# Performance work log

Measured on AMD Instinct MI355X. Metric: run time of the kernel, lower is better.

## Reference

```python
import jax, jax.numpy as jnp
import numpy as np

BIG = 1.0e6  # sentinel 'infinite' 1D distance (BIG**2 = 1e12 is safely finite in fp32)


def _edt_sq(zero_mask):
    """Exact squared Euclidean distance transform to nearest True in zero_mask.

    Two-pass separable exact EDT (matches scipy.ndimage.distance_transform_edt):
      pass 1: 1-D distance along W via forward/backward cummax scans
      pass 2: min-plus over H: D2[i,j] = min_k g2[k,j] + (i-k)^2
    zero_mask: [H, W] bool (True where the source array equals 0).
    """
    H, W = zero_mask.shape
    col = jnp.arange(W, dtype=jnp.float32)
    # index of last zero to the left / first zero to the right
    last = jax.lax.cummax(jnp.where(zero_mask, col, -BIG), axis=1)
    nxt = -jax.lax.cummax(jnp.where(zero_mask, -col, -BIG), axis=1, reverse=True)
    g = jnp.minimum(jnp.minimum(col - last, nxt - col), BIG)  # [H, W] 1-D dist
    g2 = g * g
    row = jnp.arange(H, dtype=jnp.float32)
    sq = (row[:, None] - row[None, :]) ** 2  # [H, H]
    # D2[i, j] = min_k g2[k, j] + (i - k)^2  -- exact 2-D squared EDT
    return jnp.min(g2[None, :, :] + sq[:, :, None], axis=1)


def _distance_map(mask):
    """Signed distance map: EDT(mask) - EDT(1 - mask); zeros if mask empty."""
    pos = jnp.sqrt(_edt_sq(mask == 0))   # dist of foreground px to nearest background
    neg = jnp.sqrt(_edt_sq(mask != 0))   # dist of background px to nearest foreground
    d = pos - neg
    return jnp.where(mask.sum() == 0, jnp.zeros_like(d), d)


def boundary_loss(pred, target):
    B, C, H, W = pred.shape
    masks = target.reshape(B * C, H, W)
    # sequence over B*C to keep the [H,H,W] min-plus intermediate per-image
    dmaps = jax.lax.map(_distance_map, masks).reshape(B, C, H, W)
    # sum_c mean_{b,h,w}(sig(pred_c)*d_c) / C  ==  overall mean
    return jnp.mean(jax.nn.sigmoid(pred) * dmaps)


def setup_inputs() -> dict:
    key = jax.random.key(0)
    k1, k2 = jax.random.split(key)
    pred = jax.random.normal(k1, (8, 3, 256, 256), dtype=jnp.float32)
    target = jax.random.randint(k2, (8, 3, 256, 256), 0, 2, dtype=jnp.int32)
    return {"pred": pred, "target": target}


def reference(pred, target):
    return boundary_loss(pred, target)
```

## Files before the change

kernel.cpp:

```cpp
#include <hip/hip_runtime.h>
#include <math.h>

#define NIMG 24
#define H    256
#define W    256
#define NPIX (H * W)
#define NROWS (NIMG * H)
#define CPB  8
#define LDP  9
#define GRID2 (NIMG * (W / CPB))
#define NPART GRID2
#define BIGI 1000000
#define BIGF 1.0e6f
#define CAPTHR (-5.0e5f)

__global__ void edt_rows_kernel(const int* __restrict__ tgt,
                                float* __restrict__ f) {
    const int tid  = blockIdx.x * 256 + threadIdx.x;
    const int gw   = tid >> 6;
    const int lane = tid & 63;
    const int img  = gw >> 8;
    const int row  = gw & 255;

    const int4 tv = ((const int4*)(tgt + (img << 16) + (row << 8)))[lane];
    const int c0 = lane << 2;

    const int prevw = __shfl_up(tv.w, 1, 64);
    const bool ch0 = (lane > 0) && ((tv.x != 0) != (prevw != 0));
    const bool ch1 = (tv.y != 0) != (tv.x != 0);
    const bool ch2 = (tv.z != 0) != (tv.y != 0);
    const bool ch3 = (tv.w != 0) != (tv.z != 0);

    const int a0 = ch0 ? c0     : -BIGI;
    const int a1 = ch1 ? c0 + 1 : a0;
    const int a2 = ch2 ? c0 + 2 : a1;
    const int a3 = ch3 ? c0 + 3 : a2;
    const int rb3 = ch3 ? c0 + 3 : BIGI;
    const int rb2 = ch2 ? c0 + 2 : rb3;
    const int rb1 = ch1 ? c0 + 1 : rb2;
    const int rb0 = ch0 ? c0     : rb1;

    const unsigned long long mask = __ballot(ch0 | ch1 | ch2 | ch3);
    const unsigned long long lowm = mask & ((1ULL << lane) - 1ULL);
    const unsigned long long him  = (lane < 63) ? (mask >> (lane + 1)) : 0ULL;

    const int plane = 63 - __builtin_clzll(lowm | 1ULL);
    const int sh_a  = __shfl(a3, plane & 63, 64);
    const int ex    = (lowm != 0ULL) ? sh_a : -BIGI;

    const int qlane = lane + 1 +
        (int)__builtin_ctzll(him | 0x8000000000000000ULL);
    const int sh_r  = __shfl(rb0, qlane & 63, 64);
    const int exr   = (him != 0ULL) ? sh_r : BIGI;

    const int s0 = (ex > a0) ? ex : a0;
    const int s1 = (ex > a1) ? ex : a1;
    const int s2 = (ex > a2) ? ex : a2;
    const int s3 = (ex > a3) ? ex : a3;
    const int n0 = (rb1 < exr) ? rb1 : exr;
    const int n1 = (rb2 < exr) ? rb2 : exr;
    const int n2 = (rb3 < exr) ? rb3 : exr;
    const int n3 = exr;

    auto gcalc = [](int c, int s, int n) -> int {
        int dp = c - s + 1;
        int dn = n - c;
        int g = dp < dn ? dp : dn;
        return g < BIGI ? g : BIGI;
    };
    const float g0 = (float)gcalc(c0,     s0, n0);
    const float g1 = (float)gcalc(c0 + 1, s1, n1);
    const float g2 = (float)gcalc(c0 + 2, s2, n2);
    const float g3 = (float)gcalc(c0 + 3, s3, n3);

    float4 o;
    o.x = (tv.x != 0) ? g0 : -g0;
    o.y = (tv.y != 0) ? g1 : -g1;
    o.z = (tv.z != 0) ? g2 : -g2;
    o.w = (tv.w != 0) ? g3 : -g3;
    ((float4*)(f + (img << 16) + (row << 8)))[lane] = o;
}

__global__ void edt_cols_kernel(const float* __restrict__ f,
                                const float* __restrict__ pred,
                                double* __restrict__ partials) {
    const int bid  = blockIdx.x;
    const int img  = bid >> 5;
    const int j0   = (bid & 31) << 3;
    const int t    = threadIdx.x;
    const int lane = t & 63;
    const int wid  = t >> 6;

    __shared__ float sf[H][LDP];
    __shared__ double wsum[4];
    __shared__ int nonempty;
    if (t == 0) nonempty = 0;
    __syncthreads();

    bool myne = false;
#pragma unroll
    for (int s = 0; s < 2; ++s) {
        const int id  = t + (s << 8);
        const int row = id >> 1;
        const int q   = (id & 1) << 2;
        const float4 v = *(const float4*)(f + (img << 16) + (row << 8) + j0 + q);
        sf[row][q]     = v.x;  sf[row][q + 1] = v.y;
        sf[row][q + 2] = v.z;  sf[row][q + 3] = v.w;
        myne = myne || (v.x > CAPTHR) || (v.y > CAPTHR) ||
                       (v.z > CAPTHR) || (v.w > CAPTHR);
    }
    if (myne) nonempty = 1;
    __syncthreads();
    const int flag = nonempty;

    const int c  = t & 7;
    const int r0 = (t >> 3) << 3;
    double acc = 0.0;
#pragma unroll
    for (int ii = 0; ii < 8; ++ii) {
        const int i = r0 + ii;
        const float fv = sf[i][c];
        const bool  m  = fv > 0.0f;
        const float sgn = m ? 1.0f : -1.0f;
        const float gi = fabsf(fv);
        const int  gii = (int)gi;
        int lo = i - gii; lo = lo > 0 ? lo : 0;
        int hi = i + gii; hi = hi < (H - 1) ? hi : (H - 1);

        float dm = 3.0e38f;
        float dk = (float)(i - lo);
        for (int k = lo; k <= hi; ++k) {
            const float g = fmaxf(sgn * sf[k][c], 0.0f);
            dm = fminf(dm, g * g + dk * dk);
            dk -= 1.0f;
        }

        float d = m ? sqrtf(dm) : -sqrtf(dm);
        if (!flag) d = 0.0f;
        const float p = pred[(img << 16) + (i << 8) + j0 + c];
        const float sig = 1.0f / (1.0f + expf(-p));
        acc += (double)sig * (double)d;
    }

#pragma unroll
    for (int off = 32; off > 0; off >>= 1) acc += __shfl_down(acc, off, 64);
    if (lane == 0) wsum[wid] = acc;
    __syncthreads();
    if (t == 0) partials[bid] = (wsum[0] + wsum[1]) + (wsum[2] + wsum[3]);
}

__global__ void finalize_kernel(const double* __restrict__ partials,
                                float* __restrict__ out) {
    const int t = threadIdx.x;
    double a = 0.0;
#pragma unroll
    for (int s = 0; s < NPART / 64; ++s) a += partials[t + (s << 6)];
#pragma unroll
    for (int off = 32; off > 0; off >>= 1) a += __shfl_down(a, off, 64);
    if (t == 0) out[0] = (float)(a / (double)(NIMG * NPIX));
}

extern "C" void kernel_launch(void* const* d_in, const int* in_sizes, int n_in,
                              void* d_out, int out_size, void* d_ws, size_t ws_size,
                              hipStream_t stream) {
    const float* pred = (const float*)d_in[0];
    const int*   tgt  = (const int*)d_in[1];
    float* out = (float*)d_out;

    char* ws = (char*)d_ws;
    const size_t fbytes = (size_t)NIMG * NPIX * sizeof(float);
    float*  fbuf     = (float*)(ws);
    double* partials = (double*)(ws + fbytes);

    edt_rows_kernel<<<NROWS / 4, 256, 0, stream>>>(tgt, fbuf);
    edt_cols_kernel<<<GRID2, 256, 0, stream>>>(fbuf, pred, partials);
    finalize_kernel<<<1, 64, 0, stream>>>(partials, out);
}
```

Before: 25.58 us.

## Fuse row EDT, column EDT and final reduction into one kernel with per-image barriers

Merges the three launches into one persistent-style kernel. Each block computes 8 rows of the row pass and writes them to global memory. It then waits on a per-image atomic counter barrier before running the column min-plus pass. The last block to finish does the final reduction, found through an atomic ticket. Pred is prefetched into shared memory before the barrier to hide its load latency. The aim is to remove launch overhead and inter-kernel gaps, at the cost of a memset launch, spin-wait barriers that need all 32 blocks of an image co-resident, and extra shared memory.

```diff
diff --git a/kernel.cpp b/kernel.cpp
--- a/kernel.cpp
+++ b/kernel.cpp
@@ -5,105 +5,126 @@
 #define H    256
 #define W    256
 #define NPIX (H * W)
-#define NROWS (NIMG * H)
+#define SLICES 32
+#define NBLK (NIMG * SLICES)
+#define BLKT 256
 #define CPB  8
 #define LDP  9
-#define GRID2 (NIMG * (W / CPB))
-#define NPART GRID2
 #define BIGI 1000000
-#define BIGF 1.0e6f
 #define CAPTHR (-5.0e5f)
 
-__global__ void edt_rows_kernel(const int* __restrict__ tgt,
-                                float* __restrict__ f) {
-    const int tid  = blockIdx.x * 256 + threadIdx.x;
-    const int gw   = tid >> 6;
-    const int lane = tid & 63;
-    const int img  = gw >> 8;
-    const int row  = gw & 255;
-
-    const int4 tv = ((const int4*)(tgt + (img << 16) + (row << 8)))[lane];
-    const int c0 = lane << 2;
-
-    const int prevw = __shfl_up(tv.w, 1, 64);
-    const bool ch0 = (lane > 0) && ((tv.x != 0) != (prevw != 0));
-    const bool ch1 = (tv.y != 0) != (tv.x != 0);
-    const bool ch2 = (tv.z != 0) != (tv.y != 0);
-    const bool ch3 = (tv.w != 0) != (tv.z != 0);
-
-    const int a0 = ch0 ? c0     : -BIGI;
-    const int a1 = ch1 ? c0 + 1 : a0;
-    const int a2 = ch2 ? c0 + 2 : a1;
-    const int a3 = ch3 ? c0 + 3 : a2;
-    const int rb3 = ch3 ? c0 + 3 : BIGI;
-    const int rb2 = ch2 ? c0 + 2 : rb3;
-    const int rb1 = ch1 ? c0 + 1 : rb2;
-    const int rb0 = ch0 ? c0     : rb1;
-
-    const unsigned long long mask = __ballot(ch0 | ch1 | ch2 | ch3);
-    const unsigned long long lowm = mask & ((1ULL << lane) - 1ULL);
-    const unsigned long long him  = (lane < 63) ? (mask >> (lane + 1)) : 0ULL;
-
-    const int plane = 63 - __builtin_clzll(lowm | 1ULL);
-    const int sh_a  = __shfl(a3, plane & 63, 64);
-    const int ex    = (lowm != 0ULL) ? sh_a : -BIGI;
-
-    const int qlane = lane + 1 +
-        (int)__builtin_ctzll(him | 0x8000000000000000ULL);
-    const int sh_r  = __shfl(rb0, qlane & 63, 64);
-    const int exr   = (him != 0ULL) ? sh_r : BIGI;
-
-    const int s0 = (ex > a0) ? ex : a0;
-    const int s1 = (ex > a1) ? ex : a1;
-    const int s2 = (ex > a2) ? ex : a2;
-    const int s3 = (ex > a3) ? ex : a3;
-    const int n0 = (rb1 < exr) ? rb1 : exr;
-    const int n1 = (rb2 < exr) ? rb2 : exr;
-    const int n2 = (rb3 < exr) ? rb3 : exr;
-    const int n3 = exr;
-
-    auto gcalc = [](int c, int s, int n) -> int {
-        int dp = c - s + 1;
-        int dn = n - c;
-        int g = dp < dn ? dp : dn;
-        return g < BIGI ? g : BIGI;
-    };
-    const float g0 = (float)gcalc(c0,     s0, n0);
-    const float g1 = (float)gcalc(c0 + 1, s1, n1);
-    const float g2 = (float)gcalc(c0 + 2, s2, n2);
-    const float g3 = (float)gcalc(c0 + 3, s3, n3);
-
-    float4 o;
-    o.x = (tv.x != 0) ? g0 : -g0;
-    o.y = (tv.y != 0) ? g1 : -g1;
-    o.z = (tv.z != 0) ? g2 : -g2;
-    o.w = (tv.w != 0) ? g3 : -g3;
-    ((float4*)(f + (img << 16) + (row << 8)))[lane] = o;
-}
-
-__global__ void edt_cols_kernel(const float* __restrict__ f,
-                                const float* __restrict__ pred,
-                                double* __restrict__ partials) {
+__global__ __launch_bounds__(BLKT)
+void boundary_fused_kernel(const int* __restrict__ tgt,
+                           const float* __restrict__ pred,
+                           float* __restrict__ fbuf,
+                           double* __restrict__ partials,
+                           unsigned int* __restrict__ syncw,
+                           float* __restrict__ out) {
     const int bid  = blockIdx.x;
     const int img  = bid >> 5;
-    const int j0   = (bid & 31) << 3;
+    const int grp  = bid & 31;
+    const int j0   = grp << 3;
     const int t    = threadIdx.x;
     const int lane = t & 63;
     const int wid  = t >> 6;
 
     __shared__ float sf[H][LDP];
+    __shared__ float sp[H][LDP];
     __shared__ double wsum[4];
-    __shared__ int nonempty;
+    __shared__ int nonempty, won;
     if (t == 0) nonempty = 0;
-    __syncthreads();
-
-    bool myne = false;
+
+#pragma unroll
+    for (int s = 0; s < 2; ++s) {
+        const int row = (grp << 3) + (wid << 1) + s;
+        const int4 tv = ((const int4*)(tgt + (img << 16) + (row << 8)))[lane];
+        const int c0 = lane << 2;
+
+        const int prevw = __shfl_up(tv.w, 1, 64);
+        const bool ch0 = (lane > 0) && ((tv.x != 0) != (prevw != 0));
+        const bool ch1 = (tv.y != 0) != (tv.x != 0);
+        const bool ch2 = (tv.z != 0) != (tv.y != 0);
+        const bool ch3 = (tv.w != 0) != (tv.z != 0);
+
+        const int a0 = ch0 ? c0     : -BIGI;
+        const int a1 = ch1 ? c0 + 1 : a0;
+        const int a2 = ch2 ? c0 + 2 : a1;
+        const int a3 = ch3 ? c0 + 3 : a2;
+        const int rb3 = ch3 ? c0 + 3 : BIGI;
+        const int rb2 = ch2 ? c0 + 2 : rb3;
+        const int rb1 = ch1 ? c0 + 1 : rb2;
+        const int rb0 = ch0 ? c0     : rb1;
+
+        const unsigned long long mask = __ballot(ch0 | ch1 | ch2 | ch3);
+        const unsigned long long lowm = mask & ((1ULL << lane) - 1ULL);
+        const unsigned long long him  = (lane < 63) ? (mask >> (lane + 1)) : 0ULL;
+
+        const int plane = 63 - __builtin_clzll(lowm | 1ULL);
+        const int sh_a  = __shfl(a3, plane & 63, 64);
+        const int ex    = (lowm != 0ULL) ? sh_a : -BIGI;
+
+        const int qlane = lane + 1 +
+            (int)__builtin_ctzll(him | 0x8000000000000000ULL);
+        const int sh_r  = __shfl(rb0, qlane & 63, 64);
+        const int exr   = (him != 0ULL) ? sh_r : BIGI;
+
+        const int s0 = (ex > a0) ? ex : a0;
+        const int s1 = (ex > a1) ? ex : a1;
+        const int s2 = (ex > a2) ? ex : a2;
+        const int s3 = (ex > a3) ? ex : a3;
+        const int n0 = (rb1 < exr) ? rb1 : exr;
+        const int n1 = (rb2 < exr) ? rb2 : exr;
+        const int n2 = (rb3 < exr) ? rb3 : exr;
+        const int n3 = exr;
+
+        auto gcalc = [](int c, int ss, int nn) -> int {
+            int dp = c - ss + 1;
+            int dn = nn - c;
+            int g = dp < dn ? dp : dn;
+            return g < BIGI ? g : BIGI;
+        };
+        const float g0 = (float)gcalc(c0,     s0, n0);
+        const float g1 = (float)gcalc(c0 + 1, s1, n1);
+        const float g2 = (float)gcalc(c0 + 2, s2, n2);
+        const float g3 = (float)gcalc(c0 + 3, s3, n3);
+
+        float4 o;
+        o.x = (tv.x != 0) ? g0 : -g0;
+        o.y = (tv.y != 0) ? g1 : -g1;
+        o.z = (tv.z != 0) ? g2 : -g2;
+        o.w = (tv.w != 0) ? g3 : -g3;
+        ((float4*)(fbuf + (img << 16) + (row << 8)))[lane] = o;
+    }
+
 #pragma unroll
     for (int s = 0; s < 2; ++s) {
         const int id  = t + (s << 8);
         const int row = id >> 1;
         const int q   = (id & 1) << 2;
-        const float4 v = *(const float4*)(f + (img << 16) + (row << 8) + j0 + q);
+        const float4 v = *(const float4*)(pred + (img << 16) + (row << 8) + j0 + q);
+        sp[row][q]     = v.x;  sp[row][q + 1] = v.y;
+        sp[row][q + 2] = v.z;  sp[row][q + 3] = v.w;
+    }
+
+    __syncthreads();
+    if (t == 0) {
+        __threadfence();
+        atomicAdd(&syncw[img << 4], 1u);
+        while (__hip_atomic_load(&syncw[img << 4], __ATOMIC_RELAXED,
+                                 __HIP_MEMORY_SCOPE_AGENT) < SLICES) {
+            __builtin_amdgcn_s_sleep(2);
+        }
+        __threadfence();
+    }
+    __syncthreads();
+
+    bool myne = false;
+#pragma unroll
+    for (int s = 0; s < 2; ++s) {
+        const int id  = t + (s << 8);
+        const int row = id >> 1;
+        const int q   = (id & 1) << 2;
+        const float4 v = *(const float4*)(fbuf + (img << 16) + (row << 8) + j0 + q);
         sf[row][q]     = v.x;  sf[row][q + 1] = v.y;
         sf[row][q + 2] = v.z;  sf[row][q + 3] = v.w;
         myne = myne || (v.x > CAPTHR) || (v.y > CAPTHR) ||
@@ -137,7 +158,7 @@
 
         float d = m ? sqrtf(dm) : -sqrtf(dm);
         if (!flag) d = 0.0f;
-        const float p = pred[(img << 16) + (i << 8) + j0 + c];
+        const float p = sp[i][c];
         const float sig = 1.0f / (1.0f + expf(-p));
         acc += (double)sig * (double)d;
     }
@@ -146,18 +167,23 @@
     for (int off = 32; off > 0; off >>= 1) acc += __shfl_down(acc, off, 64);
     if (lane == 0) wsum[wid] = acc;
     __syncthreads();
-    if (t == 0) partials[bid] = (wsum[0] + wsum[1]) + (wsum[2] + wsum[3]);
-}
-
-__global__ void finalize_kernel(const double* __restrict__ partials,
-                                float* __restrict__ out) {
-    const int t = threadIdx.x;
-    double a = 0.0;
-#pragma unroll
-    for (int s = 0; s < NPART / 64; ++s) a += partials[t + (s << 6)];
-#pragma unroll
-    for (int off = 32; off > 0; off >>= 1) a += __shfl_down(a, off, 64);
-    if (t == 0) out[0] = (float)(a / (double)(NIMG * NPIX));
+    if (t == 0) {
+        partials[bid] = (wsum[0] + wsum[1]) + (wsum[2] + wsum[3]);
+        __threadfence();
+        const unsigned old = atomicAdd(&syncw[NIMG << 4], 1u);
+        won = (old == (unsigned)(NBLK - 1));
+    }
+    __syncthreads();
+
+    if (won && t < 64) {
+        __threadfence();
+        double a = 0.0;
+#pragma unroll
+        for (int s = 0; s < NBLK / 64; ++s) a += partials[t + (s << 6)];
+#pragma unroll
+        for (int off = 32; off > 0; off >>= 1) a += __shfl_down(a, off, 64);
+        if (t == 0) out[0] = (float)(a / (double)(NIMG * NPIX));
+    }
 }
 
 extern "C" void kernel_launch(void* const* d_in, const int* in_sizes, int n_in,
@@ -169,10 +195,11 @@
 
     char* ws = (char*)d_ws;
     const size_t fbytes = (size_t)NIMG * NPIX * sizeof(float);
-    float*  fbuf     = (float*)(ws);
-    double* partials = (double*)(ws + fbytes);
-
-    edt_rows_kernel<<<NROWS / 4, 256, 0, stream>>>(tgt, fbuf);
-    edt_cols_kernel<<<GRID2, 256, 0, stream>>>(fbuf, pred, partials);
-    finalize_kernel<<<1, 64, 0, stream>>>(partials, out);
+    float*        fbuf     = (float*)(ws);
+    double*       partials = (double*)(ws + fbytes);
+    unsigned int* syncw    = (unsigned int*)(ws + fbytes + NBLK * sizeof(double));
+
+    hipMemsetAsync(syncw, 0, (NIMG + 1) * 64, stream);
+    boundary_fused_kernel<<<NBLK, BLKT, 0, stream>>>(tgt, pred, fbuf,
+                                                     partials, syncw, out);
 }
```

Result: slower. 90.64 us (+254.4%).

## Store row distances as int16 and fold final reduction into column kernel

Applied to the files above, without the earlier changes.

The row pass now writes signed 1-D distances as shorts, capping the no-zero case at a sentinel that the column kernel expands back to 1e6, so the intermediate buffer is half as large. The separate finalize launch is removed. The last finishing block, found through per-image and global atomic counters that the row kernel resets, now sums the partials. This cuts intermediate memory traffic and one kernel launch, at the cost of atomics and threadfences and a dependency on counter reset ordering between kernels.

```diff
diff --git a/kernel.cpp b/kernel.cpp
--- a/kernel.cpp
+++ b/kernel.cpp
@@ -7,15 +7,18 @@
 #define NPIX (H * W)
 #define NROWS (NIMG * H)
 #define CPB  8
+#define SLICES (W / CPB)
+#define NBLK2 (NIMG * SLICES)
 #define LDP  9
-#define GRID2 (NIMG * (W / CPB))
-#define NPART GRID2
 #define BIGI 1000000
-#define BIGF 1.0e6f
-#define CAPTHR (-5.0e5f)
+#define CAPS 1024
 
 __global__ void edt_rows_kernel(const int* __restrict__ tgt,
-                                float* __restrict__ f) {
+                                short* __restrict__ f,
+                                unsigned int* __restrict__ syncw) {
+    if (blockIdx.x == 0 && threadIdx.x <= NIMG)
+        syncw[threadIdx.x << 4] = 0;
+
     const int tid  = blockIdx.x * 256 + threadIdx.x;
     const int gw   = tid >> 6;
     const int lane = tid & 63;
@@ -62,28 +65,31 @@
     const int n2 = (rb3 < exr) ? rb3 : exr;
     const int n3 = exr;
 
-    auto gcalc = [](int c, int s, int n) -> int {
-        int dp = c - s + 1;
-        int dn = n - c;
+    auto gcalc = [](int c, int ss, int nn) -> int {
+        int dp = c - ss + 1;
+        int dn = nn - c;
         int g = dp < dn ? dp : dn;
-        return g < BIGI ? g : BIGI;
+        return (g < BIGI) ? g : CAPS;
     };
-    const float g0 = (float)gcalc(c0,     s0, n0);
-    const float g1 = (float)gcalc(c0 + 1, s1, n1);
-    const float g2 = (float)gcalc(c0 + 2, s2, n2);
-    const float g3 = (float)gcalc(c0 + 3, s3, n3);
+    const int g0 = gcalc(c0,     s0, n0);
+    const int g1 = gcalc(c0 + 1, s1, n1);
+    const int g2 = gcalc(c0 + 2, s2, n2);
+    const int g3 = gcalc(c0 + 3, s3, n3);
 
-    float4 o;
-    o.x = (tv.x != 0) ? g0 : -g0;
-    o.y = (tv.y != 0) ? g1 : -g1;
-    o.z = (tv.z != 0) ? g2 : -g2;
-    o.w = (tv.w != 0) ? g3 : -g3;
-    ((float4*)(f + (img << 16) + (row << 8)))[lane] = o;
+    short4 o;
+    o.x = (short)((tv.x != 0) ? g0 : -g0);
+    o.y = (short)((tv.y != 0) ? g1 : -g1);
+    o.z = (short)((tv.z != 0) ? g2 : -g2);
+    o.w = (short)((tv.w != 0) ? g3 : -g3);
+    ((short4*)(f + (img << 16) + (row << 8)))[lane] = o;
 }
 
-__global__ void edt_cols_kernel(const float* __restrict__ f,
-                                const float* __restrict__ pred,
-                                double* __restrict__ partials) {
+__global__ __launch_bounds__(256)
+void edt_cols_kernel(const short* __restrict__ f,
+                     const float* __restrict__ pred,
+                     double* __restrict__ partials,
+                     unsigned int* __restrict__ syncw,
+                     float* __restrict__ out) {
     const int bid  = blockIdx.x;
     const int img  = bid >> 5;
     const int j0   = (bid & 31) << 3;
@@ -93,23 +99,25 @@
 
     __shared__ float sf[H][LDP];
     __shared__ double wsum[4];
-    __shared__ int nonempty;
+    __shared__ int nonempty, won;
     if (t == 0) nonempty = 0;
     __syncthreads();
 
-    bool myne = false;
+    {
+        const int4 rv = *(const int4*)(f + (img << 16) + (t << 8) + j0);
+        const short* sv = (const short*)&rv;
+        bool ne = false;
 #pragma unroll
-    for (int s = 0; s < 2; ++s) {
-        const int id  = t + (s << 8);
-        const int row = id >> 1;
-        const int q   = (id & 1) << 2;
-        const float4 v = *(const float4*)(f + (img << 16) + (row << 8) + j0 + q);
-        sf[row][q]     = v.x;  sf[row][q + 1] = v.y;
-        sf[row][q + 2] = v.z;  sf[row][q + 3] = v.w;
-        myne = myne || (v.x > CAPTHR) || (v.y > CAPTHR) ||
-                       (v.z > CAPTHR) || (v.w > CAPTHR);
+        for (int j = 0; j < 8; ++j) {
+            const int v = sv[j];
+            ne = ne || (v != -CAPS);
+            float g = (float)v;
+            if (v == CAPS)  g =  1.0e6f;
+            if (v == -CAPS) g = -1.0e6f;
+            sf[t][j] = g;
+        }
+        if (ne) nonempty = 1;
     }
-    if (myne) nonempty = 1;
     __syncthreads();
     const int flag = nonempty;
 
@@ -146,18 +154,28 @@
     for (int off = 32; off > 0; off >>= 1) acc += __shfl_down(acc, off, 64);
     if (lane == 0) wsum[wid] = acc;
     __syncthreads();
-    if (t == 0) partials[bid] = (wsum[0] + wsum[1]) + (wsum[2] + wsum[3]);
-}
+    if (t == 0) {
+        partials[bid] = (wsum[0] + wsum[1]) + (wsum[2] + wsum[3]);
+        __threadfence();
+        int w = 0;
+        const unsigned o1 = atomicAdd(&syncw[img << 4], 1u);
+        if (o1 == (unsigned)(SLICES - 1)) {
+            const unsigned o2 = atomicAdd(&syncw[NIMG << 4], 1u);
+            w = (o2 == (unsigned)(NIMG - 1));
+        }
+        won = w;
+    }
+    __syncthreads();
 
-__global__ void finalize_kernel(const double* __restrict__ partials,
-                                float* __restrict__ out) {
-    const int t = threadIdx.x;
-    double a = 0.0;
+    if (won && t < 64) {
+        __threadfence();
+        double a = 0.0;
 #pragma unroll
-    for (int s = 0; s < NPART / 64; ++s) a += partials[t + (s << 6)];
+        for (int s = 0; s < NBLK2 / 64; ++s) a += partials[t + (s << 6)];
 #pragma unroll
-    for (int off = 32; off > 0; off >>= 1) a += __shfl_down(a, off, 64);
-    if (t == 0) out[0] = (float)(a / (double)(NIMG * NPIX));
+        for (int off = 32; off > 0; off >>= 1) a += __shfl_down(a, off, 64);
+        if (t == 0) out[0] = (float)(a / (double)(NIMG * NPIX));
+    }
 }
 
 extern "C" void kernel_launch(void* const* d_in, const int* in_sizes, int n_in,
@@ -168,11 +186,11 @@
     float* out = (float*)d_out;
 
     char* ws = (char*)d_ws;
-    const size_t fbytes = (size_t)NIMG * NPIX * sizeof(float);
-    float*  fbuf     = (float*)(ws);
-    double* partials = (double*)(ws + fbytes);
+    const size_t fbytes = (size_t)NIMG * NPIX * sizeof(short);
+    short*        fbuf     = (short*)(ws);
+    double*       partials = (double*)(ws + fbytes);
+    unsigned int* syncw    = (unsigned int*)(ws + fbytes + NBLK2 * sizeof(double));
 
-    edt_rows_kernel<<<NROWS / 4, 256, 0, stream>>>(tgt, fbuf);
-    edt_cols_kernel<<<GRID2, 256, 0, stream>>>(fbuf, pred, partials);
-    finalize_kernel<<<1, 64, 0, stream>>>(partials, out);
+    edt_rows_kernel<<<NROWS / 4, 256, 0, stream>>>(tgt, fbuf, syncw);
+    edt_cols_kernel<<<NBLK2, 256, 0, stream>>>(fbuf, pred, partials, syncw, out);
 }
```

After: 39.83 us. +55.7%, slower.

## Fuse row EDT pass into column kernel, recomputing rows per block

Applied to the files above, without the earlier changes.

Merges the row-distance kernel into the column min-plus kernel. Each block now reads the full target image rows and recomputes the 1-D distances, keeping only its 8-column slice in shared memory, so the intermediate float buffer round-trip and one launch disappear. The block-to-image mapping is also remapped to spread the images across the grid. The cost is redundant work: every image's row pass and the reads of its full target image are repeated by 32 blocks, so global reads grow while writes and a launch are removed.

```diff
diff --git a/kernel.cpp b/kernel.cpp
--- a/kernel.cpp
+++ b/kernel.cpp
@@ -5,88 +5,20 @@
 #define H    256
 #define W    256
 #define NPIX (H * W)
-#define NROWS (NIMG * H)
 #define CPB  8
+#define SLICES (W / CPB)
+#define NBLK (NIMG * SLICES)
 #define LDP  9
-#define GRID2 (NIMG * (W / CPB))
-#define NPART GRID2
 #define BIGI 1000000
-#define BIGF 1.0e6f
-#define CAPTHR (-5.0e5f)
 
-__global__ void edt_rows_kernel(const int* __restrict__ tgt,
-                                float* __restrict__ f) {
-    const int tid  = blockIdx.x * 256 + threadIdx.x;
-    const int gw   = tid >> 6;
-    const int lane = tid & 63;
-    const int img  = gw >> 8;
-    const int row  = gw & 255;
-
-    const int4 tv = ((const int4*)(tgt + (img << 16) + (row << 8)))[lane];
-    const int c0 = lane << 2;
-
-    const int prevw = __shfl_up(tv.w, 1, 64);
-    const bool ch0 = (lane > 0) && ((tv.x != 0) != (prevw != 0));
-    const bool ch1 = (tv.y != 0) != (tv.x != 0);
-    const bool ch2 = (tv.z != 0) != (tv.y != 0);
-    const bool ch3 = (tv.w != 0) != (tv.z != 0);
-
-    const int a0 = ch0 ? c0     : -BIGI;
-    const int a1 = ch1 ? c0 + 1 : a0;
-    const int a2 = ch2 ? c0 + 2 : a1;
-    const int a3 = ch3 ? c0 + 3 : a2;
-    const int rb3 = ch3 ? c0 + 3 : BIGI;
-    const int rb2 = ch2 ? c0 + 2 : rb3;
-    const int rb1 = ch1 ? c0 + 1 : rb2;
-    const int rb0 = ch0 ? c0     : rb1;
-
-    const unsigned long long mask = __ballot(ch0 | ch1 | ch2 | ch3);
-    const unsigned long long lowm = mask & ((1ULL << lane) - 1ULL);
-    const unsigned long long him  = (lane < 63) ? (mask >> (lane + 1)) : 0ULL;
-
-    const int plane = 63 - __builtin_clzll(lowm | 1ULL);
-    const int sh_a  = __shfl(a3, plane & 63, 64);
-    const int ex    = (lowm != 0ULL) ? sh_a : -BIGI;
-
-    const int qlane = lane + 1 +
-        (int)__builtin_ctzll(him | 0x8000000000000000ULL);
-    const int sh_r  = __shfl(rb0, qlane & 63, 64);
-    const int exr   = (him != 0ULL) ? sh_r : BIGI;
-
-    const int s0 = (ex > a0) ? ex : a0;
-    const int s1 = (ex > a1) ? ex : a1;
-    const int s2 = (ex > a2) ? ex : a2;
-    const int s3 = (ex > a3) ? ex : a3;
-    const int n0 = (rb1 < exr) ? rb1 : exr;
-    const int n1 = (rb2 < exr) ? rb2 : exr;
-    const int n2 = (rb3 < exr) ? rb3 : exr;
-    const int n3 = exr;
-
-    auto gcalc = [](int c, int s, int n) -> int {
-        int dp = c - s + 1;
-        int dn = n - c;
-        int g = dp < dn ? dp : dn;
-        return g < BIGI ? g : BIGI;
-    };
-    const float g0 = (float)gcalc(c0,     s0, n0);
-    const float g1 = (float)gcalc(c0 + 1, s1, n1);
-    const float g2 = (float)gcalc(c0 + 2, s2, n2);
-    const float g3 = (float)gcalc(c0 + 3, s3, n3);
-
-    float4 o;
-    o.x = (tv.x != 0) ? g0 : -g0;
-    o.y = (tv.y != 0) ? g1 : -g1;
-    o.z = (tv.z != 0) ? g2 : -g2;
-    o.w = (tv.w != 0) ? g3 : -g3;
-    ((float4*)(f + (img << 16) + (row << 8)))[lane] = o;
-}
-
-__global__ void edt_cols_kernel(const float* __restrict__ f,
-                                const float* __restrict__ pred,
-                                double* __restrict__ partials) {
+__global__ __launch_bounds__(256)
+void boundary_main_kernel(const int* __restrict__ tgt,
+                          const float* __restrict__ pred,
+                          double* __restrict__ partials) {
     const int bid  = blockIdx.x;
-    const int img  = bid >> 5;
-    const int j0   = (bid & 31) << 3;
+    const int img  = ((bid & 7) * 3) + (bid >> 8);
+    const int grp  = (bid >> 3) & 31;
+    const int j0   = grp << 3;
     const int t    = threadIdx.x;
     const int lane = t & 63;
     const int wid  = t >> 6;
@@ -97,19 +29,75 @@
     if (t == 0) nonempty = 0;
     __syncthreads();
 
-    bool myne = false;
-#pragma unroll
-    for (int s = 0; s < 2; ++s) {
-        const int id  = t + (s << 8);
-        const int row = id >> 1;
-        const int q   = (id & 1) << 2;
-        const float4 v = *(const float4*)(f + (img << 16) + (row << 8) + j0 + q);
-        sf[row][q]     = v.x;  sf[row][q + 1] = v.y;
-        sf[row][q + 2] = v.z;  sf[row][q + 3] = v.w;
-        myne = myne || (v.x > CAPTHR) || (v.y > CAPTHR) ||
-                       (v.z > CAPTHR) || (v.w > CAPTHR);
+    const int  c0   = lane << 2;
+    const int  cb   = c0 - j0;
+    const bool mine = (cb >= 0) && (cb < CPB);
+    const int  ibase = img << 16;
+    int anynz = 0;
+
+    for (int rr = 0; rr < 64; ++rr) {
+        const int row = (wid << 6) + rr;
+        const int4 tv = ((const int4*)(tgt + ibase + (row << 8)))[lane];
+        anynz |= tv.x | tv.y | tv.z | tv.w;
+
+        const int prevw = __shfl_up(tv.w, 1, 64);
+        const bool ch0 = (lane > 0) && ((tv.x != 0) != (prevw != 0));
+        const bool ch1 = (tv.y != 0) != (tv.x != 0);
+        const bool ch2 = (tv.z != 0) != (tv.y != 0);
+        const bool ch3 = (tv.w != 0) != (tv.z != 0);
+
+        const int a0 = ch0 ? c0     : -BIGI;
+        const int a1 = ch1 ? c0 + 1 : a0;
+        const int a2 = ch2 ? c0 + 2 : a1;
+        const int a3 = ch3 ? c0 + 3 : a2;
+        const int rb3 = ch3 ? c0 + 3 : BIGI;
+        const int rb2 = ch2 ? c0 + 2 : rb3;
+        const int rb1 = ch1 ? c0 + 1 : rb2;
+        const int rb0 = ch0 ? c0     : rb1;
+
+        const unsigned long long mask = __ballot(ch0 | ch1 | ch2 | ch3);
+        const unsigned long long lowm = mask & ((1ULL << lane) - 1ULL);
+        const unsigned long long him  = (lane < 63) ? (mask >> (lane + 1)) : 0ULL;
+
+        const int plane = 63 - __builtin_clzll(lowm | 1ULL);
+        const int sh_a  = __shfl(a3, plane & 63, 64);
+        const int ex    = (lowm != 0ULL) ? sh_a : -BIGI;
+
+        const int qlane = lane + 1 +
+            (int)__builtin_ctzll(him | 0x8000000000000000ULL);
+        const int sh_r  = __shfl(rb0, qlane & 63, 64);
+        const int exr   = (him != 0ULL) ? sh_r : BIGI;
+
+        if (mine) {
+            const int s0 = (ex > a0) ? ex : a0;
+            const int s1 = (ex > a1) ? ex : a1;
+            const int s2 = (ex > a2) ? ex : a2;
+            const int s3 = (ex > a3) ? ex : a3;
+            const int n0 = (rb1 < exr) ? rb1 : exr;
+            const int n1 = (rb2 < exr) ? rb2 : exr;
+            const int n2 = (rb3 < exr) ? rb3 : exr;
+            const int n3 = exr;
+
+            auto gcalc = [](int c, int ss, int nn) -> int {
+                int dp = c - ss + 1;
+                int dn = nn - c;
+                int g = dp < dn ? dp : dn;
+                return g < BIGI ? g : BIGI;
+            };
+            const float g0 = (float)gcalc(c0,     s0, n0);
+            const float g1 = (float)gcalc(c0 + 1, s1, n1);
+            const float g2 = (float)gcalc(c0 + 2, s2, n2);
+            const float g3 = (float)gcalc(c0 + 3, s3, n3);
+
+            sf[row][cb]     = (tv.x != 0) ? g0 : -g0;
+            sf[row][cb + 1] = (tv.y != 0) ? g1 : -g1;
+            sf[row][cb + 2] = (tv.z != 0) ? g2 : -g2;
+            sf[row][cb + 3] = (tv.w != 0) ? g3 : -g3;
+        }
     }
-    if (myne) nonempty = 1;
+    if (__any(anynz != 0)) {
+        if (lane == 0) nonempty = 1;
+    }
     __syncthreads();
     const int flag = nonempty;
 
@@ -137,7 +125,7 @@
 
         float d = m ? sqrtf(dm) : -sqrtf(dm);
         if (!flag) d = 0.0f;
-        const float p = pred[(img << 16) + (i << 8) + j0 + c];
+        const float p = pred[ibase + (i << 8) + j0 + c];
         const float sig = 1.0f / (1.0f + expf(-p));
         acc += (double)sig * (double)d;
     }
@@ -154,7 +142,7 @@
     const int t = threadIdx.x;
     double a = 0.0;
 #pragma unroll
-    for (int s = 0; s < NPART / 64; ++s) a += partials[t + (s << 6)];
+    for (int s = 0; s < NBLK / 64; ++s) a += partials[t + (s << 6)];
 #pragma unroll
     for (int off = 32; off > 0; off >>= 1) a += __shfl_down(a, off, 64);
     if (t == 0) out[0] = (float)(a / (double)(NIMG * NPIX));
@@ -167,12 +155,8 @@
     const int*   tgt  = (const int*)d_in[1];
     float* out = (float*)d_out;
 
-    char* ws = (char*)d_ws;
-    const size_t fbytes = (size_t)NIMG * NPIX * sizeof(float);
-    float*  fbuf     = (float*)(ws);
-    double* partials = (double*)(ws + fbytes);
+    double* partials = (double*)d_ws;
 
-    edt_rows_kernel<<<NROWS / 4, 256, 0, stream>>>(tgt, fbuf);
-    edt_cols_kernel<<<GRID2, 256, 0, stream>>>(fbuf, pred, partials);
+    boundary_main_kernel<<<NBLK, 256, 0, stream>>>(tgt, pred, partials);
     finalize_kernel<<<1, 64, 0, stream>>>(partials, out);
 }
```

Result: slower. 47.55 us (+85.9%).
